# Kernel optimization log

Measured on AMD Instinct MI355X. Metric: run time of the kernel, lower is better.

Reference implementation:

```python
import jax, jax.numpy as jnp
import numpy as np

MARGIN = 0.3
BIG = 10000.0  # sentinel used by the original when a gt/lt negative set is empty


def setup_inputs() -> dict:
    key = jax.random.key(0)
    k1, k2 = jax.random.split(key)
    inputs = jax.random.normal(k1, (4096, 256), dtype=jnp.float32)
    targets = jax.random.randint(k2, (4096,), 0, 4, dtype=jnp.int32)
    return {"inputs": inputs, "targets": targets}


def reference(inputs, targets):
    # Pairwise Euclidean distance matrix (n, n).
    sq = jnp.sum(inputs * inputs, axis=1)
    d2 = sq[:, None] + sq[None, :] - 2.0 * (inputs @ inputs.T)
    dist = jnp.sqrt(jnp.maximum(d2, 0.0))

    # mask[i, j] semantics from the torch code (rows of expand are `targets`):
    #   eq: targets[j] == targets[i]; gt: targets[j] > targets[i]; lt: targets[j] < targets[i]
    eq = targets[None, :] == targets[:, None]
    gt = targets[None, :] > targets[:, None]
    lt = targets[None, :] < targets[:, None]

    # Hardest positive: max distance over same-label columns (diag always eq -> non-empty).
    hard_ap = jnp.max(jnp.where(eq, dist, -jnp.inf), axis=1)
    # Hardest greater / less negatives: min distance, sentinel BIG when set empty.
    an_g = jnp.min(jnp.where(gt, dist, jnp.inf), axis=1)
    an_g = jnp.where(jnp.isinf(an_g), BIG, an_g)
    an_l = jnp.min(jnp.where(lt, dist, jnp.inf), axis=1)
    an_l = jnp.where(jnp.isinf(an_l), BIG, an_l)

    loss = jnp.mean(jax.nn.relu(hard_ap - jnp.abs(an_g - an_l) + MARGIN))
    # cnt: rows whose positive set is just the anchor itself
    cnt = jnp.sum(jnp.sum(eq, axis=1) == 1)
    return loss, dist, cnt
```

## Files before the change

kernel.cpp:

```cpp
#include <hip/hip_runtime.h>

#define N 4096
#define D 256
#define MARGIN 0.3f
#define BIG 10000.0f

typedef _Float16 f16x8 __attribute__((ext_vector_type(8)));
typedef _Float16 f16x4 __attribute__((ext_vector_type(4)));
typedef float floatx16 __attribute__((ext_vector_type(16)));

__device__ inline void atomicMaxFloatPos(float* a, float v) {
    atomicMax((int*)a, __float_as_int(v));
}
__device__ inline void atomicMinFloatPos(float* a, float v) {
    atomicMin((int*)a, __float_as_int(v));
}

__device__ inline void gl_lds16(const void* g, void* l) {
    __builtin_amdgcn_global_load_lds(
        (const __attribute__((address_space(1))) unsigned int*)g,
        (__attribute__((address_space(3))) unsigned int*)l, 16, 0, 0);
}

__global__ __launch_bounds__(256) void prep_kernel(const float* __restrict__ x,
                                                   float* __restrict__ sq,
                                                   _Float16* __restrict__ Xf,
                                                   float* ap, float* ang, float* anl,
                                                   float* __restrict__ out) {
    const int wave = threadIdx.x >> 6, lane = threadIdx.x & 63;
    const int row = blockIdx.x * 4 + wave;
    const float4 v = *(const float4*)(x + (size_t)row * D + lane * 4);
    f16x4 h;
    h[0] = (_Float16)v.x; h[1] = (_Float16)v.y;
    h[2] = (_Float16)v.z; h[3] = (_Float16)v.w;
    *(f16x4*)(Xf + (size_t)row * D + lane * 4) = h;
    const float c0 = (float)h[0], c1 = (float)h[1], c2 = (float)h[2], c3 = (float)h[3];
    float s = c0 * c0 + c1 * c1 + c2 * c2 + c3 * c3;
    #pragma unroll
    for (int off = 32; off; off >>= 1) s += __shfl_down(s, off);
    if (lane == 0) sq[row] = s;
    if (threadIdx.x < 4) {
        const int i = blockIdx.x * 4 + threadIdx.x;
        ap[i] = 0.0f; ang[i] = BIG; anl[i] = BIG;
    }
    if (blockIdx.x == 0 && threadIdx.x == 0) {
        out[0] = 0.0f;
        out[1 + (size_t)N * N] = 0.0f;
    }
}

__global__ __launch_bounds__(512, 1) void dist_kernel(const _Float16* __restrict__ Xf,
                                                      const int* __restrict__ tgt,
                                                      const float* __restrict__ sq,
                                                      float* __restrict__ dist,
                                                      float* ap, float* ang, float* anl) {
    __shared__ _Float16 lds[65536];

    const int tid  = threadIdx.x;
    const int wv   = tid >> 6;
    const int lane = tid & 63;
    const int row0 = blockIdx.y * 256;
    const int col0 = blockIdx.x * 256;
    const int wr = wv >> 2, wc = wv & 3;

    const int g = lane >> 3, p = lane & 7, lq = p ^ g;
    const int sel  = (lq < 4 ? row0 : col0) + g;
    const int koff = (lq & 3) * 8;

    const int m0 = lane & 31;
    const int hi = lane >> 5;
    const int sw = m0 & 7;

    floatx16 acc[4][2];
    #pragma unroll
    for (int mt = 0; mt < 4; ++mt)
        #pragma unroll
        for (int nt = 0; nt < 2; ++nt)
            #pragma unroll
            for (int r = 0; r < 16; ++r) acc[mt][nt][r] = 0.0f;

    #define ISSUE_STAGE(st)                                                       \
    do {                                                                          \
        _Float16* buf_ = lds + ((st) & 3) * 16384;                                \
        const int k0_ = (st) * 32;                                                \
        _Pragma("unroll")                                                         \
        for (int d = 0; d < 4; ++d) {                                             \
            const int rg = wv * 4 + d;                                            \
            gl_lds16(Xf + (size_t)(sel + rg * 8) * D + k0_ + koff,                \
                     buf_ + rg * 512);                                            \
        }                                                                         \
    } while (0)

    ISSUE_STAGE(0);
    ISSUE_STAGE(1);
    ISSUE_STAGE(2);

    #pragma unroll
    for (int s = 0; s < 8; ++s) {
        if (s < 6)      { __asm__ volatile("s_waitcnt vmcnt(8)" ::: "memory"); }
        else if (s == 6){ __asm__ volatile("s_waitcnt vmcnt(4)" ::: "memory"); }
        else            { __asm__ volatile("s_waitcnt vmcnt(0)" ::: "memory"); }
        __builtin_amdgcn_s_barrier();
        if (s < 5) ISSUE_STAGE(s + 3);

        const _Float16* buf = lds + (s & 3) * 16384;
        const _Float16* Ab  = buf + ((size_t)wr * 128 + m0) * 64;
        const _Float16* Bb  = buf + ((size_t)wc * 64  + m0) * 64;

        __builtin_amdgcn_s_setprio(1);
        #pragma unroll
        for (int ks = 0; ks < 2; ++ks) {
            const int la  = ks * 2 + hi;
            const int poa = ((la       ^ sw) << 3);
            const int pob = (((la + 4) ^ sw) << 3);
            f16x8 b0 = *(const f16x8*)(Bb + pob);
            f16x8 b1 = *(const f16x8*)(Bb + 2048 + pob);
            #pragma unroll
            for (int mt = 0; mt < 4; ++mt) {
                f16x8 a = *(const f16x8*)(Ab + mt * 2048 + poa);
                acc[mt][0] = __builtin_amdgcn_mfma_f32_32x32x16_f16(a, b0, acc[mt][0], 0, 0, 0);
                acc[mt][1] = __builtin_amdgcn_mfma_f32_32x32x16_f16(a, b1, acc[mt][1], 0, 0, 0);
            }
        }
        __builtin_amdgcn_s_setprio(0);
        __asm__ volatile("" ::: "memory");
    }
    #undef ISSUE_STAGE

    const int rowA    = row0 + wr * 128;
    const int colbase = col0 + wc * 64;
    const int tl0 = tgt[rowA + lane];
    const int tl1 = tgt[rowA + 64 + lane];
    const float sqr0 = sq[rowA + lane];
    const float sqr1 = sq[rowA + 64 + lane];
    const unsigned long long pa0 = __ballot(tl0 & 1), pa1 = __ballot(tl0 & 2);
    const unsigned long long pb0 = __ballot(tl1 & 1), pb1 = __ballot(tl1 & 2);
    const int gc0 = colbase + m0, gc1 = colbase + 32 + m0;
    const int tc0 = tgt[gc0], tc1 = tgt[gc1];
    const float sqc0 = sq[gc0], sqc1 = sq[gc1];
    const int rl_base = 4 * hi;

    float mx0 = 0.0f, mg0 = BIG, ml0 = BIG;
    float mx1 = 0.0f, mg1 = BIG, ml1 = BIG;

    #pragma unroll
    for (int mt = 0; mt < 4; ++mt) {
        #pragma unroll
        for (int r = 0; r < 16; ++r) {
            const int row_l = mt * 32 + (r & 3) + 8 * (r >> 2) + rl_base;
            const int rl = row_l & 63;
            const int grow = rowA + row_l;
            const float sqi = __shfl(mt < 2 ? sqr0 : sqr1, rl);
            const float d0 = sqrtf(fmaxf(sqi + sqc0 - 2.0f * acc[mt][0][r], 0.0f));
            const float d1 = sqrtf(fmaxf(sqi + sqc1 - 2.0f * acc[mt][1][r], 0.0f));
            dist[(size_t)grow * N + gc0] = d0;
            dist[(size_t)grow * N + gc1] = d1;
            const unsigned long long q0 = (mt < 2 ? pa0 : pb0);
            const unsigned long long q1 = (mt < 2 ? pa1 : pb1);
            const int tr = (int)((q0 >> rl) & 1) | ((int)((q1 >> rl) & 1) << 1);
            mx0 = fmaxf(mx0, (tr == tc0) ? d0 : 0.0f);
            mg0 = fminf(mg0, (tr >  tc0) ? d0 : BIG);
            ml0 = fminf(ml0, (tr <  tc0) ? d0 : BIG);
            mx1 = fmaxf(mx1, (tr == tc1) ? d1 : 0.0f);
            mg1 = fminf(mg1, (tr >  tc1) ? d1 : BIG);
            ml1 = fminf(ml1, (tr <  tc1) ? d1 : BIG);
        }
    }
    mx0 = fmaxf(mx0, __shfl_xor(mx0, 32));
    mg0 = fminf(mg0, __shfl_xor(mg0, 32));
    ml0 = fminf(ml0, __shfl_xor(ml0, 32));
    mx1 = fmaxf(mx1, __shfl_xor(mx1, 32));
    mg1 = fminf(mg1, __shfl_xor(mg1, 32));
    ml1 = fminf(ml1, __shfl_xor(ml1, 32));

    if (hi == 0) {
        atomicMaxFloatPos(&ap[gc0],  mx0);
        atomicMinFloatPos(&ang[gc0], mg0);
        atomicMinFloatPos(&anl[gc0], ml0);
        atomicMaxFloatPos(&ap[gc1],  mx1);
        atomicMinFloatPos(&ang[gc1], mg1);
        atomicMinFloatPos(&anl[gc1], ml1);
    }
}

__global__ __launch_bounds__(256) void finish_kernel(const float* __restrict__ ap,
                                                     const float* __restrict__ ang,
                                                     const float* __restrict__ anl,
                                                     const int* __restrict__ tgt,
                                                     float* __restrict__ out) {
    __shared__ unsigned hs01[4], hs23[4];
    __shared__ float fs[4];
    __shared__ int   cs[4];
    const int tid = threadIdx.x, lane = tid & 63, wv = tid >> 6;

    int c[4] = {0, 0, 0, 0};
    #pragma unroll
    for (int j = 0; j < 4; ++j) {
        const int4 t4 = *(const int4*)&tgt[(j * 256 + tid) * 4];
        c[t4.x & 3]++; c[t4.y & 3]++; c[t4.z & 3]++; c[t4.w & 3]++;
    }
    unsigned p01 = (unsigned)c[0] | ((unsigned)c[1] << 16);
    unsigned p23 = (unsigned)c[2] | ((unsigned)c[3] << 16);
    #pragma unroll
    for (int off = 32; off; off >>= 1) {
        p01 += __shfl_down(p01, off);
        p23 += __shfl_down(p23, off);
    }
    if (lane == 0) { hs01[wv] = p01; hs23[wv] = p23; }
    __syncthreads();
    const unsigned a = hs01[0] + hs01[1] + hs01[2] + hs01[3];
    const unsigned b = hs23[0] + hs23[1] + hs23[2] + hs23[3];
    const int h0 = a & 0xFFFF, h1 = a >> 16, h2 = b & 0xFFFF, h3 = b >> 16;

    const int row = blockIdx.x * 256 + tid;
    const int t = tgt[row] & 3;
    float term = fmaxf(ap[row] - fabsf(ang[row] - anl[row]) + MARGIN, 0.0f);
    const int h = (t == 0) ? h0 : (t == 1) ? h1 : (t == 2) ? h2 : h3;
    int cc = (h == 1) ? 1 : 0;

    #pragma unroll
    for (int off = 32; off; off >>= 1) {
        term += __shfl_down(term, off);
        cc   += __shfl_down(cc, off);
    }
    if (lane == 0) { fs[wv] = term; cs[wv] = cc; }
    __syncthreads();
    if (tid == 0) {
        const float ls = fs[0] + fs[1] + fs[2] + fs[3];
        const int   csum = cs[0] + cs[1] + cs[2] + cs[3];
        atomicAdd(&out[0], ls * (1.0f / N));
        atomicAdd(&out[1 + (size_t)N * N], (float)csum);
    }
}

extern "C" void kernel_launch(void* const* d_in, const int* in_sizes, int n_in,
                              void* d_out, int out_size, void* d_ws, size_t ws_size,
                              hipStream_t stream) {
    const float* x   = (const float*)d_in[0];
    const int*   tgt = (const int*)d_in[1];
    float* out = (float*)d_out;
    char*  ws  = (char*)d_ws;

    _Float16* Xf  = (_Float16*)ws;
    float*    sq  = (float*)(ws + 2097152);
    float*    ap  = sq + 4096;
    float*    ang = sq + 8192;
    float*    anl = sq + 12288;

    prep_kernel<<<N / 4, 256, 0, stream>>>(x, sq, Xf, ap, ang, anl, out);
    dim3 grid(N / 256, N / 256);
    dist_kernel<<<grid, 512, 0, stream>>>(Xf, tgt, sq, out + 1, ap, ang, anl);
    finish_kernel<<<16, 256, 0, stream>>>(ap, ang, anl, tgt, out);
}
```

Before: 102.6 us.

## Shrink distance tiles to 128x128 with 4 waves and three-stage LDS ring

Reduces the distance-kernel output tile from 256x256 with 8 waves to 128x128 with 4 waves. Each wave now holds a 64x64 accumulator, and the LDS pipeline drops from four stages to three, which cuts shared memory per block to 48 KB. The grid grows from 256 to 1024 blocks and launch bounds allow 3 blocks per CU, so the 256 CUs get better occupancy and load balance. In exchange, operand reuse per loaded byte is lower, the prefetch depth is shorter, and each column gets more atomic reductions.

```diff
diff --git a/kernel.cpp b/kernel.cpp
--- a/kernel.cpp
+++ b/kernel.cpp
@@ -49,19 +49,19 @@
     }
 }
 
-__global__ __launch_bounds__(512, 1) void dist_kernel(const _Float16* __restrict__ Xf,
+__global__ __launch_bounds__(256, 3) void dist_kernel(const _Float16* __restrict__ Xf,
                                                       const int* __restrict__ tgt,
                                                       const float* __restrict__ sq,
                                                       float* __restrict__ dist,
                                                       float* ap, float* ang, float* anl) {
-    __shared__ _Float16 lds[65536];
+    __shared__ _Float16 lds[24576];
 
     const int tid  = threadIdx.x;
     const int wv   = tid >> 6;
     const int lane = tid & 63;
-    const int row0 = blockIdx.y * 256;
-    const int col0 = blockIdx.x * 256;
-    const int wr = wv >> 2, wc = wv & 3;
+    const int row0 = blockIdx.y * 128;
+    const int col0 = blockIdx.x * 128;
+    const int wr = wv >> 1, wc = wv & 1;
 
     const int g = lane >> 3, p = lane & 7, lq = p ^ g;
     const int sel  = (lq < 4 ? row0 : col0) + g;
@@ -71,9 +71,9 @@
     const int hi = lane >> 5;
     const int sw = m0 & 7;
 
-    floatx16 acc[4][2];
-    #pragma unroll
-    for (int mt = 0; mt < 4; ++mt)
+    floatx16 acc[2][2];
+    #pragma unroll
+    for (int mt = 0; mt < 2; ++mt)
         #pragma unroll
         for (int nt = 0; nt < 2; ++nt)
             #pragma unroll
@@ -81,7 +81,7 @@
 
     #define ISSUE_STAGE(st)                                                       \
     do {                                                                          \
-        _Float16* buf_ = lds + ((st) & 3) * 16384;                                \
+        _Float16* buf_ = lds + ((st) % 3) * 8192;                                 \
         const int k0_ = (st) * 32;                                                \
         _Pragma("unroll")                                                         \
         for (int d = 0; d < 4; ++d) {                                             \
@@ -93,19 +93,17 @@
 
     ISSUE_STAGE(0);
     ISSUE_STAGE(1);
-    ISSUE_STAGE(2);
 
     #pragma unroll
     for (int s = 0; s < 8; ++s) {
-        if (s < 6)      { __asm__ volatile("s_waitcnt vmcnt(8)" ::: "memory"); }
-        else if (s == 6){ __asm__ volatile("s_waitcnt vmcnt(4)" ::: "memory"); }
-        else            { __asm__ volatile("s_waitcnt vmcnt(0)" ::: "memory"); }
+        if (s < 7) { __asm__ volatile("s_waitcnt vmcnt(4)" ::: "memory"); }
+        else       { __asm__ volatile("s_waitcnt vmcnt(0)" ::: "memory"); }
         __builtin_amdgcn_s_barrier();
-        if (s < 5) ISSUE_STAGE(s + 3);
-
-        const _Float16* buf = lds + (s & 3) * 16384;
-        const _Float16* Ab  = buf + ((size_t)wr * 128 + m0) * 64;
-        const _Float16* Bb  = buf + ((size_t)wc * 64  + m0) * 64;
+        if (s < 6) ISSUE_STAGE(s + 2);
+
+        const _Float16* buf = lds + (s % 3) * 8192;
+        const _Float16* Ab  = buf + ((size_t)wr * 64 + m0) * 64;
+        const _Float16* Bb  = buf + ((size_t)wc * 64 + m0) * 64;
 
         __builtin_amdgcn_s_setprio(1);
         #pragma unroll
@@ -113,28 +111,26 @@
             const int la  = ks * 2 + hi;
             const int poa = ((la       ^ sw) << 3);
             const int pob = (((la + 4) ^ sw) << 3);
+            f16x8 a0 = *(const f16x8*)(Ab + poa);
+            f16x8 a1 = *(const f16x8*)(Ab + 2048 + poa);
             f16x8 b0 = *(const f16x8*)(Bb + pob);
             f16x8 b1 = *(const f16x8*)(Bb + 2048 + pob);
-            #pragma unroll
-            for (int mt = 0; mt < 4; ++mt) {
-                f16x8 a = *(const f16x8*)(Ab + mt * 2048 + poa);
-                acc[mt][0] = __builtin_amdgcn_mfma_f32_32x32x16_f16(a, b0, acc[mt][0], 0, 0, 0);
-                acc[mt][1] = __builtin_amdgcn_mfma_f32_32x32x16_f16(a, b1, acc[mt][1], 0, 0, 0);
-            }
+            acc[0][0] = __builtin_amdgcn_mfma_f32_32x32x16_f16(a0, b0, acc[0][0], 0, 0, 0);
+            acc[0][1] = __builtin_amdgcn_mfma_f32_32x32x16_f16(a0, b1, acc[0][1], 0, 0, 0);
+            acc[1][0] = __builtin_amdgcn_mfma_f32_32x32x16_f16(a1, b0, acc[1][0], 0, 0, 0);
+            acc[1][1] = __builtin_amdgcn_mfma_f32_32x32x16_f16(a1, b1, acc[1][1], 0, 0, 0);
         }
         __builtin_amdgcn_s_setprio(0);
         __asm__ volatile("" ::: "memory");
     }
     #undef ISSUE_STAGE
 
-    const int rowA    = row0 + wr * 128;
+    const int rowbase = row0 + wr * 64;
     const int colbase = col0 + wc * 64;
-    const int tl0 = tgt[rowA + lane];
-    const int tl1 = tgt[rowA + 64 + lane];
-    const float sqr0 = sq[rowA + lane];
-    const float sqr1 = sq[rowA + 64 + lane];
-    const unsigned long long pa0 = __ballot(tl0 & 1), pa1 = __ballot(tl0 & 2);
-    const unsigned long long pb0 = __ballot(tl1 & 1), pb1 = __ballot(tl1 & 2);
+    const int tl = tgt[rowbase + lane];
+    const float sq_r = sq[rowbase + lane];
+    const unsigned long long pb_0 = __ballot(tl & 1);
+    const unsigned long long pb_1 = __ballot(tl & 2);
     const int gc0 = colbase + m0, gc1 = colbase + 32 + m0;
     const int tc0 = tgt[gc0], tc1 = tgt[gc1];
     const float sqc0 = sq[gc0], sqc1 = sq[gc1];
@@ -144,20 +140,17 @@
     float mx1 = 0.0f, mg1 = BIG, ml1 = BIG;
 
     #pragma unroll
-    for (int mt = 0; mt < 4; ++mt) {
+    for (int mt = 0; mt < 2; ++mt) {
         #pragma unroll
         for (int r = 0; r < 16; ++r) {
             const int row_l = mt * 32 + (r & 3) + 8 * (r >> 2) + rl_base;
-            const int rl = row_l & 63;
-            const int grow = rowA + row_l;
-            const float sqi = __shfl(mt < 2 ? sqr0 : sqr1, rl);
+            const int grow  = rowbase + row_l;
+            const float sqi = __shfl(sq_r, row_l);
             const float d0 = sqrtf(fmaxf(sqi + sqc0 - 2.0f * acc[mt][0][r], 0.0f));
             const float d1 = sqrtf(fmaxf(sqi + sqc1 - 2.0f * acc[mt][1][r], 0.0f));
             dist[(size_t)grow * N + gc0] = d0;
             dist[(size_t)grow * N + gc1] = d1;
-            const unsigned long long q0 = (mt < 2 ? pa0 : pb0);
-            const unsigned long long q1 = (mt < 2 ? pa1 : pb1);
-            const int tr = (int)((q0 >> rl) & 1) | ((int)((q1 >> rl) & 1) << 1);
+            const int tr = (int)((pb_0 >> row_l) & 1) | ((int)((pb_1 >> row_l) & 1) << 1);
             mx0 = fmaxf(mx0, (tr == tc0) ? d0 : 0.0f);
             mg0 = fminf(mg0, (tr >  tc0) ? d0 : BIG);
             ml0 = fminf(ml0, (tr <  tc0) ? d0 : BIG);
@@ -248,7 +241,7 @@
     float*    anl = sq + 12288;
 
     prep_kernel<<<N / 4, 256, 0, stream>>>(x, sq, Xf, ap, ang, anl, out);
-    dim3 grid(N / 256, N / 256);
-    dist_kernel<<<grid, 512, 0, stream>>>(Xf, tgt, sq, out + 1, ap, ang, anl);
+    dim3 grid(N / 128, N / 128);
+    dist_kernel<<<grid, 256, 0, stream>>>(Xf, tgt, sq, out + 1, ap, ang, anl);
     finish_kernel<<<16, 256, 0, stream>>>(ap, ang, anl, tgt, out);
 }
```

After: 103.4 us. No clear change (+0.8%).
